# Performance work log

Hardware: AMD Instinct MI355X
Metric: run time of the kernel (lower is better)

Reference implementation:

```python
import jax, jax.numpy as jnp
import numpy as np

B, S, D_IN, D_OUT, H = 2, 2048, 1024, 1024, 16
DK = D_OUT // H


def setup_inputs() -> dict:
    key = jax.random.key(0)
    ks = jax.random.split(key, 6)
    s_in = 1.0 / np.sqrt(D_IN)
    s_out = 1.0 / np.sqrt(D_OUT)
    return {
        "x": jax.random.normal(ks[0], (B, S, D_IN), dtype=jnp.float32),
        "Wq": jax.random.uniform(ks[1], (D_OUT, D_IN), jnp.float32, -s_in, s_in),
        "Wk": jax.random.uniform(ks[2], (D_OUT, D_IN), jnp.float32, -s_in, s_in),
        "Wv": jax.random.uniform(ks[3], (D_OUT, D_IN), jnp.float32, -s_in, s_in),
        "Wo": jax.random.uniform(ks[4], (D_OUT, D_OUT), jnp.float32, -s_out, s_out),
        "bo": jax.random.uniform(ks[5], (D_OUT,), jnp.float32, -s_out, s_out),
    }


def reference(x, Wq, Wk, Wv, Wo, bo):
    b, s, _ = x.shape
    # torch Linear: y = x @ W.T
    q = (x @ Wq.T).reshape(b, s, H, DK).transpose(0, 2, 1, 3)  # [b,h,s,dk]
    k = (x @ Wk.T).reshape(b, s, H, DK).transpose(0, 2, 1, 3)
    v = (x @ Wv.T).reshape(b, s, H, DK).transpose(0, 2, 1, 3)
    scores = jnp.einsum("bhqd,bhkd->bhqk", q, k)
    causal = jnp.tril(jnp.ones((s, s), dtype=bool))  # True = keep
    scores = jnp.where(causal, scores, -jnp.inf)
    attn = jax.nn.softmax(scores / np.sqrt(DK), axis=-1)
    # dropout p=0.0 (eval) -> identity
    ctx = jnp.einsum("bhqk,bhkd->bhqd", attn, v)
    ctx = ctx.transpose(0, 2, 1, 3).reshape(b, s, D_OUT)
    return ctx @ Wo.T + bo
```

## Files before the change

### kernel.cpp

```cpp
#include <hip/hip_runtime.h>
#include <stdint.h>

#define B_   2
#define S_   2048
#define DIN  1024
#define DOUT 1024
#define H_   16
#define DK_  64
#define MSZ  (B_ * S_)

typedef __bf16 bf16v8 __attribute__((ext_vector_type(8)));
typedef float  f32x4  __attribute__((ext_vector_type(4)));

__device__ __forceinline__ ushort f2b(float f) {
  union { float f; uint32_t u; } a; a.f = f;
  uint32_t u = a.u;
  u += 0x7FFFu + ((u >> 16) & 1u);
  return (ushort)(u >> 16);
}

__device__ __forceinline__ uint32_t pk2(float lo, float hi) {
  union { __bf16 h; ushort u; } a, b;
  a.h = (__bf16)lo; b.h = (__bf16)hi;
  return (uint32_t)a.u | ((uint32_t)b.u << 16);
}

#define GLDS(gp, lp) __builtin_amdgcn_global_load_lds(                         \
    (const __attribute__((address_space(1))) void*)(gp),                       \
    (__attribute__((address_space(3))) void*)(lp), 16, 0, 0)

__global__ void cvt_all(const float* __restrict__ x,  const float* __restrict__ wq,
                        const float* __restrict__ wk, const float* __restrict__ wv,
                        const float* __restrict__ wo,
                        ushort* __restrict__ xb,  ushort* __restrict__ wqb,
                        ushort* __restrict__ wkb, ushort* __restrict__ wvb,
                        ushort* __restrict__ wob) {
  int i = blockIdx.x * blockDim.x + threadIdx.x;
  const int NX = 1 << 20, NW = 1 << 18;
  const float* src; ushort* dst; int off;
  if (i < NX)               { src = x;  dst = xb;  off = i; }
  else if (i < NX + NW)     { src = wq; dst = wqb; off = i - NX; }
  else if (i < NX + 2 * NW) { src = wk; dst = wkb; off = i - NX - NW; }
  else if (i < NX + 3 * NW) { src = wv; dst = wvb; off = i - NX - 2 * NW; }
  else                      { src = wo; dst = wob; off = i - NX - 3 * NW; }
  float4 v = reinterpret_cast<const float4*>(src)[off];
  ushort4 o;
  o.x = f2b(v.x); o.y = f2b(v.y); o.z = f2b(v.z); o.w = f2b(v.w);
  reinterpret_cast<ushort4*>(dst)[off] = o;
}

template<int MODE>
__global__ __launch_bounds__(256)
void gemm_nt(const ushort* __restrict__ A,
             const ushort* __restrict__ Bq, const ushort* __restrict__ Bk,
             const ushort* __restrict__ Bv,
             ushort* __restrict__ Oq, ushort* __restrict__ Ok,
             ushort* __restrict__ Vt,
             float* __restrict__ Cf, const float* __restrict__ bias,
             int M, int N, int K) {
  __shared__ ushort sA[128 * 32];
  __shared__ ushort sB[128 * 32];

  const int tid  = threadIdx.x;
  const int lane = tid & 63, wid = tid >> 6;
  const int wr = wid >> 1, wc = wid & 1;
  const int g = lane >> 4, c = lane & 15;
  const int m0 = blockIdx.x * 128, n0 = blockIdx.y * 128;

  const ushort* Bm = Bq;
  ushort* Ob = nullptr;
  float oscale = 1.0f;
  bool tv = false;
  if (MODE == 0) {
    int z = blockIdx.z;
    Bm = (z == 0) ? Bq : (z == 1) ? Bk : Bv;
    Ob = (z == 0) ? Oq : Ok;
    tv = (z == 2);
    if (z == 0) oscale = 0.125f * 1.4426950408889634f;
  }

  f32x4 acc[4][4] = {};

  for (int k0 = 0; k0 < K; k0 += 32) {
    __syncthreads();
#pragma unroll
    for (int i = 0; i < 2; ++i) {
      int o   = (i * 256 + tid) * 16;
      int row = o >> 6;
      int cb  = o & 63;
      const ushort* ga = A  + (size_t)(m0 + row) * K + k0 + (cb >> 1);
      GLDS(ga, (char*)sA + o);
      const ushort* gb = Bm + (size_t)(n0 + row) * K + k0 + (cb >> 1);
      GLDS(gb, (char*)sB + o);
    }
    __syncthreads();

    bf16v8 aF[4], bF[4];
#pragma unroll
    for (int m = 0; m < 4; ++m)
      aF[m] = *reinterpret_cast<const bf16v8*>(&sA[(wr * 64 + m * 16 + c) * 32 + g * 8]);
#pragma unroll
    for (int n = 0; n < 4; ++n)
      bF[n] = *reinterpret_cast<const bf16v8*>(&sB[(wc * 64 + n * 16 + c) * 32 + g * 8]);
#pragma unroll
    for (int m = 0; m < 4; ++m)
#pragma unroll
      for (int n = 0; n < 4; ++n)
        acc[m][n] = __builtin_amdgcn_mfma_f32_16x16x32_bf16(aF[m], bF[n], acc[m][n], 0, 0, 0);
  }

  const int rbase = m0 + wr * 64 + g * 4;
  const int cbase = n0 + wc * 64 + c;
#pragma unroll
  for (int m = 0; m < 4; ++m) {
#pragma unroll
    for (int n = 0; n < 4; ++n) {
      int col = cbase + n * 16;
      if (MODE == 1) {
        float bv = bias[col];
#pragma unroll
        for (int i = 0; i < 4; ++i)
          Cf[(size_t)(rbase + m * 16 + i) * N + col] = acc[m][n][i] + bv;
      } else if (tv) {
        int row0 = rbase + m * 16;
        int bb = row0 >> 11, ss = row0 & 2047;
        int hh = col >> 6, dd = col & 63;
        ushort4 o4;
        o4.x = f2b(acc[m][n][0]); o4.y = f2b(acc[m][n][1]);
        o4.z = f2b(acc[m][n][2]); o4.w = f2b(acc[m][n][3]);
        *reinterpret_cast<ushort4*>(
            &Vt[((size_t)(bb * 16 + hh) * 64 + dd) * 2048 + ss]) = o4;
      } else {
#pragma unroll
        for (int i = 0; i < 4; ++i)
          Ob[(size_t)(rbase + m * 16 + i) * N + col] = f2b(acc[m][n][i] * oscale);
      }
    }
  }
}

__global__ __launch_bounds__(256)
void flash_attn(const ushort* __restrict__ Q, const ushort* __restrict__ K,
                const ushort* __restrict__ Vt, ushort* __restrict__ O) {
  __shared__ ushort sK[2][64][64];
  __shared__ ushort sV[2][64][64];
  __shared__ ushort sP[4][16][64];

  const int tid  = threadIdx.x;
  const int lane = tid & 63, wid = tid >> 6;
  const int g = lane >> 4, c = lane & 15;
  const int bh = blockIdx.x;
  const int qta = blockIdx.y;
  const int qtb = (S_ / 64 - 1) - qta;
  const int b = bh >> 4, h = bh & 15;
  const int q0a = qta * 64, q0b = qtb * 64;

  const ushort* Qb = Q  + (size_t)b * S_ * DOUT + h * DK_;
  const ushort* Kb = K  + (size_t)b * S_ * DOUT + h * DK_;
  const ushort* Vb = Vt + (size_t)bh * DK_ * S_;

  const int sr   = lane >> 3;
  const int swc  = ((lane & 7) ^ sr) << 3;
  const int row0 = wid * 8 + sr;
  const int msk  = (c & 7) << 4;
  const int pswz = (c & 7) << 2;

  bf16v8 qfa[2], qfb[2];
  {
    const ushort* qa = Qb + (size_t)(q0a + wid * 16 + c) * DOUT;
    const ushort* qb2 = Qb + (size_t)(q0b + wid * 16 + c) * DOUT;
    qfa[0] = *reinterpret_cast<const bf16v8*>(qa + g * 8);
    qfa[1] = *reinterpret_cast<const bf16v8*>(qa + 32 + g * 8);
    qfb[0] = *reinterpret_cast<const bf16v8*>(qb2 + g * 8);
    qfb[1] = *reinterpret_cast<const bf16v8*>(qb2 + 32 + g * 8);
  }

  bf16v8 ones;
#pragma unroll
  for (int j = 0; j < 8; ++j) ones[j] = (__bf16)1.0f;

#pragma unroll
  for (int j = 0; j < 2; ++j) {
    int r = j * 32 + row0;
    GLDS(Kb + (size_t)r * DOUT + swc,
         (char*)&sK[0][0][0] + (j * 32 + wid * 8) * 128 + lane * 16);
    GLDS(Vb + (size_t)r * S_ + swc,
         (char*)&sV[0][0][0] + (j * 32 + wid * 8) * 128 + lane * 16);
  }
  __syncthreads();

  f32x4 accOa[4] = {}, accOb[4] = {};
  f32x4 accLa = {}, accLb = {};
  char* sPw = (char*)&sP[wid][0][0];

  int buf = 0;
  for (int kv0 = 0; kv0 <= q0b; kv0 += 64, buf ^= 1) {
    if (kv0 + 64 <= q0b) {
      const int nb = buf ^ 1, kvn = kv0 + 64;
#pragma unroll
      for (int j = 0; j < 2; ++j) {
        int r = j * 32 + row0;
        GLDS(Kb + (size_t)(kvn + r) * DOUT + swc,
             (char*)&sK[nb][0][0] + (j * 32 + wid * 8) * 128 + lane * 16);
        GLDS(Vb + (size_t)r * S_ + kvn + swc,
             (char*)&sV[nb][0][0] + (j * 32 + wid * 8) * 128 + lane * 16);
      }
    }

    const char* cK = (const char*)&sK[buf][0][0];
    const char* cV = (const char*)&sV[buf][0][0];

    auto tile = [&](const bf16v8* qf, f32x4* accO, f32x4& accL, int q0x) {
      f32x4 s[4] = {};
#pragma unroll
      for (int nf = 0; nf < 4; ++nf) {
        const char* rp = cK + (nf * 16 + c) * 128;
#pragma unroll
        for (int ks = 0; ks < 2; ++ks) {
          bf16v8 kf = *reinterpret_cast<const bf16v8*>(rp + ((ks * 64 + g * 16) ^ msk));
          s[nf] = __builtin_amdgcn_mfma_f32_16x16x32_bf16(kf, qf[ks], s[nf], 0, 0, 0);
        }
      }
      if (kv0 + 63 > q0x + wid * 16) {
        const int qg = q0x + wid * 16 + c;
#pragma unroll
        for (int nf = 0; nf < 4; ++nf)
#pragma unroll
          for (int i = 0; i < 4; ++i)
            if (kv0 + nf * 16 + g * 4 + i > qg) s[nf][i] = -1e30f;
      }
#pragma unroll
      for (int nf = 0; nf < 4; ++nf) {
        float p0 = exp2f(s[nf][0]), p1 = exp2f(s[nf][1]);
        float p2 = exp2f(s[nf][2]), p3 = exp2f(s[nf][3]);
        uint2 w2; w2.x = pk2(p0, p1); w2.y = pk2(p2, p3);
        *reinterpret_cast<uint2*>(
            sPw + c * 128 + (((nf * 8 + g * 2) ^ pswz) << 2)) = w2;
      }
      bf16v8 pf[2];
#pragma unroll
      for (int ks = 0; ks < 2; ++ks)
        pf[ks] = *reinterpret_cast<const bf16v8*>(
            sPw + c * 128 + (((ks * 16 + g * 4) ^ pswz) << 2));
#pragma unroll
      for (int ks = 0; ks < 2; ++ks)
        accL = __builtin_amdgcn_mfma_f32_16x16x32_bf16(pf[ks], ones, accL, 0, 0, 0);
#pragma unroll
      for (int nf2 = 0; nf2 < 4; ++nf2) {
        const char* vp = cV + (nf2 * 16 + c) * 128;
#pragma unroll
        for (int ks = 0; ks < 2; ++ks) {
          bf16v8 vf = *reinterpret_cast<const bf16v8*>(vp + ((ks * 64 + g * 16) ^ msk));
          accO[nf2] = __builtin_amdgcn_mfma_f32_16x16x32_bf16(pf[ks], vf, accO[nf2], 0, 0, 0);
        }
      }
    };

    if (kv0 <= q0a) tile(qfa, accOa, accLa, q0a);
    tile(qfb, accOb, accLb, q0b);

    __syncthreads();
  }

  auto epi = [&](f32x4* accO, f32x4& accL, int q0x) {
#pragma unroll
    for (int nf = 0; nf < 4; ++nf)
#pragma unroll
      for (int i = 0; i < 4; ++i) {
        int prow = g * 4 + i;
        float v = accO[nf][i] / accL[i];
        *(ushort*)(sPw + prow * 128 +
                   ((nf * 32 + c * 2) ^ ((prow & 7) << 4))) = f2b(v);
      }
    const int r = lane >> 2, cq = lane & 3;
    const char* base = sPw + r * 128;
    const int m2 = (r & 7) << 4;
    bf16v8 t0 = *reinterpret_cast<const bf16v8*>(base + ((cq * 32) ^ m2));
    bf16v8 t1 = *reinterpret_cast<const bf16v8*>(base + ((cq * 32 + 16) ^ m2));
    ushort* Gb = O + (size_t)b * S_ * DOUT +
                 (size_t)(q0x + wid * 16 + r) * DOUT + h * DK_ + cq * 16;
    *reinterpret_cast<bf16v8*>(Gb) = t0;
    *reinterpret_cast<bf16v8*>(Gb + 8) = t1;
  };
  epi(accOa, accLa, q0a);
  epi(accOb, accLb, q0b);
}

extern "C" void kernel_launch(void* const* d_in, const int* in_sizes, int n_in,
                              void* d_out, int out_size, void* d_ws, size_t ws_size,
                              hipStream_t stream) {
  const float* x  = (const float*)d_in[0];
  const float* Wq = (const float*)d_in[1];
  const float* Wk = (const float*)d_in[2];
  const float* Wv = (const float*)d_in[3];
  const float* Wo = (const float*)d_in[4];
  const float* bo = (const float*)d_in[5];
  float* out = (float*)d_out;

  char* ws = (char*)d_ws;
  const size_t MB = (size_t)1 << 20;
  ushort* xb  = (ushort*)(ws);
  ushort* wqb = (ushort*)(ws +  8 * MB);
  ushort* wkb = (ushort*)(ws + 10 * MB);
  ushort* wvb = (ushort*)(ws + 12 * MB);
  ushort* wob = (ushort*)(ws + 14 * MB);
  ushort* qb  = (ushort*)(ws + 16 * MB);
  ushort* kb  = (ushort*)(ws + 24 * MB);
  ushort* vtb = (ushort*)(ws + 32 * MB);
  ushort* cb  = (ushort*)(ws);

  const int ncv = (1 << 20) + 4 * (1 << 18);
  cvt_all<<<ncv / 256, 256, 0, stream>>>(x, Wq, Wk, Wv, Wo,
                                         xb, wqb, wkb, wvb, wob);

  dim3 gqkv(MSZ / 128, DOUT / 128, 3);
  gemm_nt<0><<<gqkv, 256, 0, stream>>>(xb, wqb, wkb, wvb, qb, kb, vtb,
                                       nullptr, nullptr, MSZ, DOUT, DIN);

  dim3 gattn(B_ * H_, S_ / 128);
  flash_attn<<<gattn, 256, 0, stream>>>(qb, kb, vtb, cb);

  dim3 gproj(MSZ / 128, DOUT / 128, 1);
  gemm_nt<1><<<gproj, 256, 0, stream>>>(cb, wob, nullptr, nullptr,
                                        nullptr, nullptr, nullptr, out, bo,
                                        MSZ, DOUT, DOUT);
}
```

Before: 120.7 us.

## Rewrite flash attention to read K/V directly from global with XCD-aware scheduling

Drops the LDS double-buffered K/V staging and has each wave load its K and V MFMA fragments straight from global memory, relying on L2 for reuse. This removes the __syncthreads barriers and the LDS traffic. Each block now handles one 64-row query tile, using a 1D grid remapped so that all tiles of one batch-head land on the same XCD and the heaviest causal tiles are scheduled first. s_setprio is added around the MFMA sections. The cost is redundant global/L2 loads across the four waves and the loss of the paired-tile load balancing.

```diff
diff --git a/kernel.cpp b/kernel.cpp
--- a/kernel.cpp
+++ b/kernel.cpp
@@ -142,148 +142,115 @@
 __global__ __launch_bounds__(256)
 void flash_attn(const ushort* __restrict__ Q, const ushort* __restrict__ K,
                 const ushort* __restrict__ Vt, ushort* __restrict__ O) {
-  __shared__ ushort sK[2][64][64];
-  __shared__ ushort sV[2][64][64];
   __shared__ ushort sP[4][16][64];
 
   const int tid  = threadIdx.x;
   const int lane = tid & 63, wid = tid >> 6;
   const int g = lane >> 4, c = lane & 15;
-  const int bh = blockIdx.x;
-  const int qta = blockIdx.y;
-  const int qtb = (S_ / 64 - 1) - qta;
+
+  const int orig = blockIdx.x;
+  const int xcd  = orig & 7, idc = orig >> 3;
+  const int bh   = xcd * 4 + (idc >> 5);
+  const int qt   = 31 - (idc & 31);
   const int b = bh >> 4, h = bh & 15;
-  const int q0a = qta * 64, q0b = qtb * 64;
+  const int q0 = qt * 64;
 
   const ushort* Qb = Q  + (size_t)b * S_ * DOUT + h * DK_;
   const ushort* Kb = K  + (size_t)b * S_ * DOUT + h * DK_;
   const ushort* Vb = Vt + (size_t)bh * DK_ * S_;
 
-  const int sr   = lane >> 3;
-  const int swc  = ((lane & 7) ^ sr) << 3;
-  const int row0 = wid * 8 + sr;
-  const int msk  = (c & 7) << 4;
   const int pswz = (c & 7) << 2;
 
-  bf16v8 qfa[2], qfb[2];
+  bf16v8 qf[2];
   {
-    const ushort* qa = Qb + (size_t)(q0a + wid * 16 + c) * DOUT;
-    const ushort* qb2 = Qb + (size_t)(q0b + wid * 16 + c) * DOUT;
-    qfa[0] = *reinterpret_cast<const bf16v8*>(qa + g * 8);
-    qfa[1] = *reinterpret_cast<const bf16v8*>(qa + 32 + g * 8);
-    qfb[0] = *reinterpret_cast<const bf16v8*>(qb2 + g * 8);
-    qfb[1] = *reinterpret_cast<const bf16v8*>(qb2 + 32 + g * 8);
+    const ushort* qrow = Qb + (size_t)(q0 + wid * 16 + c) * DOUT;
+    qf[0] = *reinterpret_cast<const bf16v8*>(qrow + g * 8);
+    qf[1] = *reinterpret_cast<const bf16v8*>(qrow + 32 + g * 8);
   }
 
   bf16v8 ones;
 #pragma unroll
   for (int j = 0; j < 8; ++j) ones[j] = (__bf16)1.0f;
 
-#pragma unroll
-  for (int j = 0; j < 2; ++j) {
-    int r = j * 32 + row0;
-    GLDS(Kb + (size_t)r * DOUT + swc,
-         (char*)&sK[0][0][0] + (j * 32 + wid * 8) * 128 + lane * 16);
-    GLDS(Vb + (size_t)r * S_ + swc,
-         (char*)&sV[0][0][0] + (j * 32 + wid * 8) * 128 + lane * 16);
-  }
-  __syncthreads();
-
-  f32x4 accOa[4] = {}, accOb[4] = {};
-  f32x4 accLa = {}, accLb = {};
+  const ushort* Kl = Kb + (size_t)c * DOUT + g * 8;
+  const ushort* Vl = Vb + (size_t)c * S_ + g * 8;
+
+  f32x4 accO[4] = {};
+  f32x4 accL = {};
   char* sPw = (char*)&sP[wid][0][0];
-
-  int buf = 0;
-  for (int kv0 = 0; kv0 <= q0b; kv0 += 64, buf ^= 1) {
-    if (kv0 + 64 <= q0b) {
-      const int nb = buf ^ 1, kvn = kv0 + 64;
-#pragma unroll
-      for (int j = 0; j < 2; ++j) {
-        int r = j * 32 + row0;
-        GLDS(Kb + (size_t)(kvn + r) * DOUT + swc,
-             (char*)&sK[nb][0][0] + (j * 32 + wid * 8) * 128 + lane * 16);
-        GLDS(Vb + (size_t)r * S_ + kvn + swc,
-             (char*)&sV[nb][0][0] + (j * 32 + wid * 8) * 128 + lane * 16);
-      }
-    }
-
-    const char* cK = (const char*)&sK[buf][0][0];
-    const char* cV = (const char*)&sV[buf][0][0];
-
-    auto tile = [&](const bf16v8* qf, f32x4* accO, f32x4& accL, int q0x) {
-      f32x4 s[4] = {};
-#pragma unroll
-      for (int nf = 0; nf < 4; ++nf) {
-        const char* rp = cK + (nf * 16 + c) * 128;
-#pragma unroll
-        for (int ks = 0; ks < 2; ++ks) {
-          bf16v8 kf = *reinterpret_cast<const bf16v8*>(rp + ((ks * 64 + g * 16) ^ msk));
-          s[nf] = __builtin_amdgcn_mfma_f32_16x16x32_bf16(kf, qf[ks], s[nf], 0, 0, 0);
-        }
-      }
-      if (kv0 + 63 > q0x + wid * 16) {
-        const int qg = q0x + wid * 16 + c;
-#pragma unroll
-        for (int nf = 0; nf < 4; ++nf)
-#pragma unroll
-          for (int i = 0; i < 4; ++i)
-            if (kv0 + nf * 16 + g * 4 + i > qg) s[nf][i] = -1e30f;
-      }
-#pragma unroll
-      for (int nf = 0; nf < 4; ++nf) {
-        float p0 = exp2f(s[nf][0]), p1 = exp2f(s[nf][1]);
-        float p2 = exp2f(s[nf][2]), p3 = exp2f(s[nf][3]);
-        uint2 w2; w2.x = pk2(p0, p1); w2.y = pk2(p2, p3);
-        *reinterpret_cast<uint2*>(
-            sPw + c * 128 + (((nf * 8 + g * 2) ^ pswz) << 2)) = w2;
-      }
-      bf16v8 pf[2];
-#pragma unroll
-      for (int ks = 0; ks < 2; ++ks)
-        pf[ks] = *reinterpret_cast<const bf16v8*>(
-            sPw + c * 128 + (((ks * 16 + g * 4) ^ pswz) << 2));
-#pragma unroll
-      for (int ks = 0; ks < 2; ++ks)
-        accL = __builtin_amdgcn_mfma_f32_16x16x32_bf16(pf[ks], ones, accL, 0, 0, 0);
-#pragma unroll
-      for (int nf2 = 0; nf2 < 4; ++nf2) {
-        const char* vp = cV + (nf2 * 16 + c) * 128;
-#pragma unroll
-        for (int ks = 0; ks < 2; ++ks) {
-          bf16v8 vf = *reinterpret_cast<const bf16v8*>(vp + ((ks * 64 + g * 16) ^ msk));
-          accO[nf2] = __builtin_amdgcn_mfma_f32_16x16x32_bf16(pf[ks], vf, accO[nf2], 0, 0, 0);
-        }
-      }
-    };
-
-    if (kv0 <= q0a) tile(qfa, accOa, accLa, q0a);
-    tile(qfb, accOb, accLb, q0b);
-
-    __syncthreads();
-  }
-
-  auto epi = [&](f32x4* accO, f32x4& accL, int q0x) {
-#pragma unroll
-    for (int nf = 0; nf < 4; ++nf)
-#pragma unroll
-      for (int i = 0; i < 4; ++i) {
-        int prow = g * 4 + i;
-        float v = accO[nf][i] / accL[i];
-        *(ushort*)(sPw + prow * 128 +
-                   ((nf * 32 + c * 2) ^ ((prow & 7) << 4))) = f2b(v);
-      }
+  const int qg = q0 + wid * 16 + c;
+  const int qdiag = q0 + wid * 16;
+
+  for (int kv0 = 0; kv0 <= q0; kv0 += 64) {
+    f32x4 s[4] = {};
+    __builtin_amdgcn_s_setprio(1);
+#pragma unroll
+    for (int nf = 0; nf < 4; ++nf) {
+      const ushort* kp = Kl + (size_t)(kv0 + nf * 16) * DOUT;
+      bf16v8 kf0 = *reinterpret_cast<const bf16v8*>(kp);
+      bf16v8 kf1 = *reinterpret_cast<const bf16v8*>(kp + 32);
+      s[nf] = __builtin_amdgcn_mfma_f32_16x16x32_bf16(kf0, qf[0], s[nf], 0, 0, 0);
+      s[nf] = __builtin_amdgcn_mfma_f32_16x16x32_bf16(kf1, qf[1], s[nf], 0, 0, 0);
+    }
+    __builtin_amdgcn_s_setprio(0);
+
+    if (kv0 + 63 > qdiag) {
+#pragma unroll
+      for (int nf = 0; nf < 4; ++nf)
+#pragma unroll
+        for (int i = 0; i < 4; ++i)
+          if (kv0 + nf * 16 + g * 4 + i > qg) s[nf][i] = -1e30f;
+    }
+
+#pragma unroll
+    for (int nf = 0; nf < 4; ++nf) {
+      float p0 = exp2f(s[nf][0]), p1 = exp2f(s[nf][1]);
+      float p2 = exp2f(s[nf][2]), p3 = exp2f(s[nf][3]);
+      uint2 w2; w2.x = pk2(p0, p1); w2.y = pk2(p2, p3);
+      *reinterpret_cast<uint2*>(
+          sPw + c * 128 + (((nf * 8 + g * 2) ^ pswz) << 2)) = w2;
+    }
+    bf16v8 pf[2];
+#pragma unroll
+    for (int ks = 0; ks < 2; ++ks)
+      pf[ks] = *reinterpret_cast<const bf16v8*>(
+          sPw + c * 128 + (((ks * 16 + g * 4) ^ pswz) << 2));
+
+    __builtin_amdgcn_s_setprio(1);
+#pragma unroll
+    for (int ks = 0; ks < 2; ++ks)
+      accL = __builtin_amdgcn_mfma_f32_16x16x32_bf16(pf[ks], ones, accL, 0, 0, 0);
+#pragma unroll
+    for (int nf2 = 0; nf2 < 4; ++nf2) {
+      const ushort* vp = Vl + (size_t)(nf2 * 16) * S_ + kv0;
+      bf16v8 vf0 = *reinterpret_cast<const bf16v8*>(vp);
+      bf16v8 vf1 = *reinterpret_cast<const bf16v8*>(vp + 32);
+      accO[nf2] = __builtin_amdgcn_mfma_f32_16x16x32_bf16(pf[0], vf0, accO[nf2], 0, 0, 0);
+      accO[nf2] = __builtin_amdgcn_mfma_f32_16x16x32_bf16(pf[1], vf1, accO[nf2], 0, 0, 0);
+    }
+    __builtin_amdgcn_s_setprio(0);
+  }
+
+#pragma unroll
+  for (int nf = 0; nf < 4; ++nf)
+#pragma unroll
+    for (int i = 0; i < 4; ++i) {
+      int prow = g * 4 + i;
+      float v = accO[nf][i] / accL[i];
+      *(ushort*)(sPw + prow * 128 +
+                 ((nf * 32 + c * 2) ^ ((prow & 7) << 4))) = f2b(v);
+    }
+  {
     const int r = lane >> 2, cq = lane & 3;
     const char* base = sPw + r * 128;
     const int m2 = (r & 7) << 4;
     bf16v8 t0 = *reinterpret_cast<const bf16v8*>(base + ((cq * 32) ^ m2));
     bf16v8 t1 = *reinterpret_cast<const bf16v8*>(base + ((cq * 32 + 16) ^ m2));
     ushort* Gb = O + (size_t)b * S_ * DOUT +
-                 (size_t)(q0x + wid * 16 + r) * DOUT + h * DK_ + cq * 16;
+                 (size_t)(q0 + wid * 16 + r) * DOUT + h * DK_ + cq * 16;
     *reinterpret_cast<bf16v8*>(Gb) = t0;
     *reinterpret_cast<bf16v8*>(Gb + 8) = t1;
-  };
-  epi(accOa, accLa, q0a);
-  epi(accOb, accLb, q0b);
+  }
 }
 
 extern "C" void kernel_launch(void* const* d_in, const int* in_sizes, int n_in,
@@ -317,8 +284,7 @@
   gemm_nt<0><<<gqkv, 256, 0, stream>>>(xb, wqb, wkb, wvb, qb, kb, vtb,
                                        nullptr, nullptr, MSZ, DOUT, DIN);
 
-  dim3 gattn(B_ * H_, S_ / 128);
-  flash_attn<<<gattn, 256, 0, stream>>>(qb, kb, vtb, cb);
+  flash_attn<<<B_ * H_ * (S_ / 64), 256, 0, stream>>>(qb, kb, vtb, cb);
 
   dim3 gproj(MSZ / 128, DOUT / 128, 1);
   gemm_nt<1><<<gproj, 256, 0, stream>>>(cb, wob, nullptr, nullptr,
```

Result: slower. 301.4 us (+149.7%).

## Remap flash-attention blocks to adjacent query tiles with XCD grouping and priority hints

Applied to the files above, without the earlier changes.

Replaces the balanced pairing of query tiles (qta, 31-qta) with pairs of adjacent tiles, so each block streams K/V only up to its own causal limit instead of the longer tile's full range. A 1D grid is remapped so each XCD handles a fixed set of heads (for L2 reuse of K/V) and the heaviest blocks are issued first. It also gives each tile its own P scratch area in shared memory, adds s_setprio around the MFMA sections, and sets a 2-blocks-per-CU launch bound. The trade is uneven work per block, which relies on heavy-first ordering to keep the tail short.

```diff
diff --git a/kernel.cpp b/kernel.cpp
--- a/kernel.cpp
+++ b/kernel.cpp
@@ -139,21 +139,23 @@
   }
 }
 
-__global__ __launch_bounds__(256)
+__global__ __launch_bounds__(256, 2)
 void flash_attn(const ushort* __restrict__ Q, const ushort* __restrict__ K,
                 const ushort* __restrict__ Vt, ushort* __restrict__ O) {
   __shared__ ushort sK[2][64][64];
   __shared__ ushort sV[2][64][64];
-  __shared__ ushort sP[4][16][64];
+  __shared__ ushort sP[8][16][64];
 
   const int tid  = threadIdx.x;
   const int lane = tid & 63, wid = tid >> 6;
   const int g = lane >> 4, c = lane & 15;
-  const int bh = blockIdx.x;
-  const int qta = blockIdx.y;
-  const int qtb = (S_ / 64 - 1) - qta;
+
+  const int orig = blockIdx.x;
+  const int xcd  = orig & 7, idc = orig >> 3;
+  const int bh   = xcd * 4 + (idc >> 4);
+  const int tp   = 15 - (idc & 15);
   const int b = bh >> 4, h = bh & 15;
-  const int q0a = qta * 64, q0b = qtb * 64;
+  const int q0a = (2 * tp) * 64, q0b = q0a + 64;
 
   const ushort* Qb = Q  + (size_t)b * S_ * DOUT + h * DK_;
   const ushort* Kb = K  + (size_t)b * S_ * DOUT + h * DK_;
@@ -167,7 +169,7 @@
 
   bf16v8 qfa[2], qfb[2];
   {
-    const ushort* qa = Qb + (size_t)(q0a + wid * 16 + c) * DOUT;
+    const ushort* qa  = Qb + (size_t)(q0a + wid * 16 + c) * DOUT;
     const ushort* qb2 = Qb + (size_t)(q0b + wid * 16 + c) * DOUT;
     qfa[0] = *reinterpret_cast<const bf16v8*>(qa + g * 8);
     qfa[1] = *reinterpret_cast<const bf16v8*>(qa + 32 + g * 8);
@@ -191,7 +193,8 @@
 
   f32x4 accOa[4] = {}, accOb[4] = {};
   f32x4 accLa = {}, accLb = {};
-  char* sPw = (char*)&sP[wid][0][0];
+  char* sPa = (char*)&sP[wid][0][0];
+  char* sPb = (char*)&sP[4 + wid][0][0];
 
   int buf = 0;
   for (int kv0 = 0; kv0 <= q0b; kv0 += 64, buf ^= 1) {
@@ -210,8 +213,10 @@
     const char* cK = (const char*)&sK[buf][0][0];
     const char* cV = (const char*)&sV[buf][0][0];
 
-    auto tile = [&](const bf16v8* qf, f32x4* accO, f32x4& accL, int q0x) {
+    auto tile = [&](const bf16v8* qf, f32x4* accO, f32x4& accL, int q0x,
+                    char* sPt) {
       f32x4 s[4] = {};
+      __builtin_amdgcn_s_setprio(1);
 #pragma unroll
       for (int nf = 0; nf < 4; ++nf) {
         const char* rp = cK + (nf * 16 + c) * 128;
@@ -221,6 +226,7 @@
           s[nf] = __builtin_amdgcn_mfma_f32_16x16x32_bf16(kf, qf[ks], s[nf], 0, 0, 0);
         }
       }
+      __builtin_amdgcn_s_setprio(0);
       if (kv0 + 63 > q0x + wid * 16) {
         const int qg = q0x + wid * 16 + c;
 #pragma unroll
@@ -229,19 +235,21 @@
           for (int i = 0; i < 4; ++i)
             if (kv0 + nf * 16 + g * 4 + i > qg) s[nf][i] = -1e30f;
       }
+      char* pbase = sPt + c * 128;
 #pragma unroll
       for (int nf = 0; nf < 4; ++nf) {
         float p0 = exp2f(s[nf][0]), p1 = exp2f(s[nf][1]);
         float p2 = exp2f(s[nf][2]), p3 = exp2f(s[nf][3]);
         uint2 w2; w2.x = pk2(p0, p1); w2.y = pk2(p2, p3);
         *reinterpret_cast<uint2*>(
-            sPw + c * 128 + (((nf * 8 + g * 2) ^ pswz) << 2)) = w2;
+            pbase + (((nf * 8 + g * 2) ^ pswz) << 2)) = w2;
       }
       bf16v8 pf[2];
 #pragma unroll
       for (int ks = 0; ks < 2; ++ks)
         pf[ks] = *reinterpret_cast<const bf16v8*>(
-            sPw + c * 128 + (((ks * 16 + g * 4) ^ pswz) << 2));
+            pbase + (((ks * 16 + g * 4) ^ pswz) << 2));
+      __builtin_amdgcn_s_setprio(1);
 #pragma unroll
       for (int ks = 0; ks < 2; ++ks)
         accL = __builtin_amdgcn_mfma_f32_16x16x32_bf16(pf[ks], ones, accL, 0, 0, 0);
@@ -254,26 +262,27 @@
           accO[nf2] = __builtin_amdgcn_mfma_f32_16x16x32_bf16(pf[ks], vf, accO[nf2], 0, 0, 0);
         }
       }
+      __builtin_amdgcn_s_setprio(0);
     };
 
-    if (kv0 <= q0a) tile(qfa, accOa, accLa, q0a);
-    tile(qfb, accOb, accLb, q0b);
+    if (kv0 <= q0a) tile(qfa, accOa, accLa, q0a, sPa);
+    tile(qfb, accOb, accLb, q0b, sPb);
 
     __syncthreads();
   }
 
-  auto epi = [&](f32x4* accO, f32x4& accL, int q0x) {
+  auto epi = [&](f32x4* accO, f32x4& accL, int q0x, char* sPt) {
 #pragma unroll
     for (int nf = 0; nf < 4; ++nf)
 #pragma unroll
       for (int i = 0; i < 4; ++i) {
         int prow = g * 4 + i;
         float v = accO[nf][i] / accL[i];
-        *(ushort*)(sPw + prow * 128 +
+        *(ushort*)(sPt + prow * 128 +
                    ((nf * 32 + c * 2) ^ ((prow & 7) << 4))) = f2b(v);
       }
     const int r = lane >> 2, cq = lane & 3;
-    const char* base = sPw + r * 128;
+    const char* base = sPt + r * 128;
     const int m2 = (r & 7) << 4;
     bf16v8 t0 = *reinterpret_cast<const bf16v8*>(base + ((cq * 32) ^ m2));
     bf16v8 t1 = *reinterpret_cast<const bf16v8*>(base + ((cq * 32 + 16) ^ m2));
@@ -282,8 +291,8 @@
     *reinterpret_cast<bf16v8*>(Gb) = t0;
     *reinterpret_cast<bf16v8*>(Gb + 8) = t1;
   };
-  epi(accOa, accLa, q0a);
-  epi(accOb, accLb, q0b);
+  epi(accOa, accLa, q0a, sPa);
+  epi(accOb, accLb, q0b, sPb);
 }
 
 extern "C" void kernel_launch(void* const* d_in, const int* in_sizes, int n_in,
@@ -317,8 +326,7 @@
   gemm_nt<0><<<gqkv, 256, 0, stream>>>(xb, wqb, wkb, wvb, qb, kb, vtb,
                                        nullptr, nullptr, MSZ, DOUT, DIN);
 
-  dim3 gattn(B_ * H_, S_ / 128);
-  flash_attn<<<gattn, 256, 0, stream>>>(qb, kb, vtb, cb);
+  flash_attn<<<B_ * H_ * (S_ / 128), 256, 0, stream>>>(qb, kb, vtb, cb);
 
   dim3 gproj(MSZ / 128, DOUT / 128, 1);
   gemm_nt<1><<<gproj, 256, 0, stream>>>(cb, wob, nullptr, nullptr,
```

After: 142.5 us. 1.18x slower.

## Split paired causal q-tiles into separate blocks with XCD-aware heavy-first ordering

Applied to the files above, without the earlier changes.

Each attention block now handles one 64-row query tile instead of a balanced pair of light and heavy tiles. A 1D grid is remapped so that blocks landing on the same XCD share (batch, head) for K/V cache locality, and the longest-running tiles are scheduled first. s_setprio is raised around the MFMA sections. This doubles the block count and drops the pairing's K/V reuse between the two tiles in exchange for better occupancy, tail balance and L2 locality.

```diff
diff --git a/kernel.cpp b/kernel.cpp
--- a/kernel.cpp
+++ b/kernel.cpp
@@ -149,11 +149,15 @@
   const int tid  = threadIdx.x;
   const int lane = tid & 63, wid = tid >> 6;
   const int g = lane >> 4, c = lane & 15;
-  const int bh = blockIdx.x;
-  const int qta = blockIdx.y;
-  const int qtb = (S_ / 64 - 1) - qta;
+
+  const int orig = blockIdx.x;
+  const int xcd  = orig & 7, d = orig >> 3;
+  int qt, hoff;
+  if (d < 64) { qt = 31 - (d >> 1); hoff = d & 1; }
+  else        { int e = d - 64; qt = e >> 1; hoff = 2 + (e & 1); }
+  const int bh = xcd * 4 + hoff;
   const int b = bh >> 4, h = bh & 15;
-  const int q0a = qta * 64, q0b = qtb * 64;
+  const int q0 = qt * 64;
 
   const ushort* Qb = Q  + (size_t)b * S_ * DOUT + h * DK_;
   const ushort* Kb = K  + (size_t)b * S_ * DOUT + h * DK_;
@@ -165,14 +169,11 @@
   const int msk  = (c & 7) << 4;
   const int pswz = (c & 7) << 2;
 
-  bf16v8 qfa[2], qfb[2];
+  bf16v8 qf[2];
   {
-    const ushort* qa = Qb + (size_t)(q0a + wid * 16 + c) * DOUT;
-    const ushort* qb2 = Qb + (size_t)(q0b + wid * 16 + c) * DOUT;
-    qfa[0] = *reinterpret_cast<const bf16v8*>(qa + g * 8);
-    qfa[1] = *reinterpret_cast<const bf16v8*>(qa + 32 + g * 8);
-    qfb[0] = *reinterpret_cast<const bf16v8*>(qb2 + g * 8);
-    qfb[1] = *reinterpret_cast<const bf16v8*>(qb2 + 32 + g * 8);
+    const ushort* qrow = Qb + (size_t)(q0 + wid * 16 + c) * DOUT;
+    qf[0] = *reinterpret_cast<const bf16v8*>(qrow + g * 8);
+    qf[1] = *reinterpret_cast<const bf16v8*>(qrow + 32 + g * 8);
   }
 
   bf16v8 ones;
@@ -189,13 +190,15 @@
   }
   __syncthreads();
 
-  f32x4 accOa[4] = {}, accOb[4] = {};
-  f32x4 accLa = {}, accLb = {};
+  f32x4 accO[4] = {};
+  f32x4 accL = {};
   char* sPw = (char*)&sP[wid][0][0];
+  const int qg = q0 + wid * 16 + c;
+  const int qdiag = q0 + wid * 16;
 
   int buf = 0;
-  for (int kv0 = 0; kv0 <= q0b; kv0 += 64, buf ^= 1) {
-    if (kv0 + 64 <= q0b) {
+  for (int kv0 = 0; kv0 <= q0; kv0 += 64, buf ^= 1) {
+    if (kv0 + 64 <= q0) {
       const int nb = buf ^ 1, kvn = kv0 + 64;
 #pragma unroll
       for (int j = 0; j < 2; ++j) {
@@ -210,80 +213,79 @@
     const char* cK = (const char*)&sK[buf][0][0];
     const char* cV = (const char*)&sV[buf][0][0];
 
-    auto tile = [&](const bf16v8* qf, f32x4* accO, f32x4& accL, int q0x) {
-      f32x4 s[4] = {};
-#pragma unroll
-      for (int nf = 0; nf < 4; ++nf) {
-        const char* rp = cK + (nf * 16 + c) * 128;
-#pragma unroll
-        for (int ks = 0; ks < 2; ++ks) {
-          bf16v8 kf = *reinterpret_cast<const bf16v8*>(rp + ((ks * 64 + g * 16) ^ msk));
-          s[nf] = __builtin_amdgcn_mfma_f32_16x16x32_bf16(kf, qf[ks], s[nf], 0, 0, 0);
-        }
+    f32x4 s[4] = {};
+    __builtin_amdgcn_s_setprio(1);
+#pragma unroll
+    for (int nf = 0; nf < 4; ++nf) {
+      const char* rp = cK + (nf * 16 + c) * 128;
+#pragma unroll
+      for (int ks = 0; ks < 2; ++ks) {
+        bf16v8 kf = *reinterpret_cast<const bf16v8*>(rp + ((ks * 64 + g * 16) ^ msk));
+        s[nf] = __builtin_amdgcn_mfma_f32_16x16x32_bf16(kf, qf[ks], s[nf], 0, 0, 0);
       }
-      if (kv0 + 63 > q0x + wid * 16) {
-        const int qg = q0x + wid * 16 + c;
-#pragma unroll
-        for (int nf = 0; nf < 4; ++nf)
-#pragma unroll
-          for (int i = 0; i < 4; ++i)
-            if (kv0 + nf * 16 + g * 4 + i > qg) s[nf][i] = -1e30f;
+    }
+    __builtin_amdgcn_s_setprio(0);
+
+    if (kv0 + 63 > qdiag) {
+#pragma unroll
+      for (int nf = 0; nf < 4; ++nf)
+#pragma unroll
+        for (int i = 0; i < 4; ++i)
+          if (kv0 + nf * 16 + g * 4 + i > qg) s[nf][i] = -1e30f;
+    }
+
+#pragma unroll
+    for (int nf = 0; nf < 4; ++nf) {
+      float p0 = exp2f(s[nf][0]), p1 = exp2f(s[nf][1]);
+      float p2 = exp2f(s[nf][2]), p3 = exp2f(s[nf][3]);
+      uint2 w2; w2.x = pk2(p0, p1); w2.y = pk2(p2, p3);
+      *reinterpret_cast<uint2*>(
+          sPw + c * 128 + (((nf * 8 + g * 2) ^ pswz) << 2)) = w2;
+    }
+    bf16v8 pf[2];
+#pragma unroll
+    for (int ks = 0; ks < 2; ++ks)
+      pf[ks] = *reinterpret_cast<const bf16v8*>(
+          sPw + c * 128 + (((ks * 16 + g * 4) ^ pswz) << 2));
+
+    __builtin_amdgcn_s_setprio(1);
+#pragma unroll
+    for (int ks = 0; ks < 2; ++ks)
+      accL = __builtin_amdgcn_mfma_f32_16x16x32_bf16(pf[ks], ones, accL, 0, 0, 0);
+#pragma unroll
+    for (int nf2 = 0; nf2 < 4; ++nf2) {
+      const char* vp = cV + (nf2 * 16 + c) * 128;
+#pragma unroll
+      for (int ks = 0; ks < 2; ++ks) {
+        bf16v8 vf = *reinterpret_cast<const bf16v8*>(vp + ((ks * 64 + g * 16) ^ msk));
+        accO[nf2] = __builtin_amdgcn_mfma_f32_16x16x32_bf16(pf[ks], vf, accO[nf2], 0, 0, 0);
       }
-#pragma unroll
-      for (int nf = 0; nf < 4; ++nf) {
-        float p0 = exp2f(s[nf][0]), p1 = exp2f(s[nf][1]);
-        float p2 = exp2f(s[nf][2]), p3 = exp2f(s[nf][3]);
-        uint2 w2; w2.x = pk2(p0, p1); w2.y = pk2(p2, p3);
-        *reinterpret_cast<uint2*>(
-            sPw + c * 128 + (((nf * 8 + g * 2) ^ pswz) << 2)) = w2;
-      }
-      bf16v8 pf[2];
-#pragma unroll
-      for (int ks = 0; ks < 2; ++ks)
-        pf[ks] = *reinterpret_cast<const bf16v8*>(
-            sPw + c * 128 + (((ks * 16 + g * 4) ^ pswz) << 2));
-#pragma unroll
-      for (int ks = 0; ks < 2; ++ks)
-        accL = __builtin_amdgcn_mfma_f32_16x16x32_bf16(pf[ks], ones, accL, 0, 0, 0);
-#pragma unroll
-      for (int nf2 = 0; nf2 < 4; ++nf2) {
-        const char* vp = cV + (nf2 * 16 + c) * 128;
-#pragma unroll
-        for (int ks = 0; ks < 2; ++ks) {
-          bf16v8 vf = *reinterpret_cast<const bf16v8*>(vp + ((ks * 64 + g * 16) ^ msk));
-          accO[nf2] = __builtin_amdgcn_mfma_f32_16x16x32_bf16(pf[ks], vf, accO[nf2], 0, 0, 0);
-        }
-      }
-    };
-
-    if (kv0 <= q0a) tile(qfa, accOa, accLa, q0a);
-    tile(qfb, accOb, accLb, q0b);
+    }
+    __builtin_amdgcn_s_setprio(0);
 
     __syncthreads();
   }
 
-  auto epi = [&](f32x4* accO, f32x4& accL, int q0x) {
-#pragma unroll
-    for (int nf = 0; nf < 4; ++nf)
-#pragma unroll
-      for (int i = 0; i < 4; ++i) {
-        int prow = g * 4 + i;
-        float v = accO[nf][i] / accL[i];
-        *(ushort*)(sPw + prow * 128 +
-                   ((nf * 32 + c * 2) ^ ((prow & 7) << 4))) = f2b(v);
-      }
+#pragma unroll
+  for (int nf = 0; nf < 4; ++nf)
+#pragma unroll
+    for (int i = 0; i < 4; ++i) {
+      int prow = g * 4 + i;
+      float v = accO[nf][i] / accL[i];
+      *(ushort*)(sPw + prow * 128 +
+                 ((nf * 32 + c * 2) ^ ((prow & 7) << 4))) = f2b(v);
+    }
+  {
     const int r = lane >> 2, cq = lane & 3;
     const char* base = sPw + r * 128;
     const int m2 = (r & 7) << 4;
     bf16v8 t0 = *reinterpret_cast<const bf16v8*>(base + ((cq * 32) ^ m2));
     bf16v8 t1 = *reinterpret_cast<const bf16v8*>(base + ((cq * 32 + 16) ^ m2));
     ushort* Gb = O + (size_t)b * S_ * DOUT +
-                 (size_t)(q0x + wid * 16 + r) * DOUT + h * DK_ + cq * 16;
+                 (size_t)(q0 + wid * 16 + r) * DOUT + h * DK_ + cq * 16;
     *reinterpret_cast<bf16v8*>(Gb) = t0;
     *reinterpret_cast<bf16v8*>(Gb + 8) = t1;
-  };
-  epi(accOa, accLa, q0a);
-  epi(accOb, accLb, q0b);
+  }
 }
 
 extern "C" void kernel_launch(void* const* d_in, const int* in_sizes, int n_in,
@@ -317,8 +319,7 @@
   gemm_nt<0><<<gqkv, 256, 0, stream>>>(xb, wqb, wkb, wvb, qb, kb, vtb,
                                        nullptr, nullptr, MSZ, DOUT, DIN);
 
-  dim3 gattn(B_ * H_, S_ / 128);
-  flash_attn<<<gattn, 256, 0, stream>>>(qb, kb, vtb, cb);
+  flash_attn<<<B_ * H_ * (S_ / 64), 256, 0, stream>>>(qb, kb, vtb, cb);
 
   dim3 gproj(MSZ / 128, DOUT / 128, 1);
   gemm_nt<1><<<gproj, 256, 0, stream>>>(cb, wob, nullptr, nullptr,
```

Result: slower. 126.2 us (+4.5%).
